# Kernel tuning notes

Hardware: AMD Instinct MI355X
Metric: run time of the kernel (lower is better)

The kernel has to match this reference:

```python
import jax, jax.numpy as jnp
import numpy as np

B, I, O, N = 65536, 256, 32, 8


def chebyshev_basis(x, n):
    """Chebyshev polynomials T_0..T_{n-1} of x. x: [B, I] -> [B, I, n]."""
    T = [jnp.ones_like(x), x]
    for _ in range(n - 2):
        T.append(2.0 * x * T[-1] - T[-2])
    return jnp.stack(T[:n], axis=-1)


def setup_inputs() -> dict:
    key = jax.random.key(0)
    k1, k2 = jax.random.split(key)
    # inputs live on [-1, 1], the natural Chebyshev domain
    x = jax.random.uniform(k1, (B, I), jnp.float32, minval=-1.0, maxval=1.0)
    # weight init mirrors torch: uniform(-weight_magnitude/in, weight_magnitude/in)
    w = jax.random.uniform(k2, (O, I, N), jnp.float32, minval=-1.0 / I, maxval=1.0 / I)
    return {"x": x, "w": w}


def reference(x, w):
    n = w.shape[-1]
    phi = chebyshev_basis(x, n)          # [B, I, n] basis expansion
    out = jnp.einsum("bin,oin->bo", phi, w)  # weighted contraction
    return out
```

## Files before the change

### kernel.cpp

```cpp
#include <hip/hip_runtime.h>
#include <hip/hip_bf16.h>


typedef __attribute__((ext_vector_type(8)))  short bf16x8;
typedef __attribute__((ext_vector_type(16))) float f32x16;
typedef __attribute__((ext_vector_type(4)))  float f32x4;

__device__ __forceinline__ short f2b(float f) {
    __hip_bfloat16 h = __float2bfloat16(f);
    short s;
    __builtin_memcpy(&s, &h, sizeof(s));
    return s;
}

__device__ __forceinline__ unsigned pkbf(float lo, float hi) {
    __hip_bfloat162 h2 = __float22bfloat162_rn(make_float2(lo, hi));
    unsigned u;
    __builtin_memcpy(&u, &h2, 4);
    return u;
}

__global__ __launch_bounds__(256) void prep_w_kernel(const float* __restrict__ w,
                                                     short* __restrict__ wB) {
    int idx = blockIdx.x * 256 + threadIdx.x;
    int kc2 = idx >> 9;
    int l   = (idx >> 3) & 63;
    int jj  = idx & 7;
    int o = l & 31, g = l >> 5;
    int i = 2 * kc2 + (jj >> 2);
    int n = 4 * g + (jj & 3);
    wB[idx] = f2b(w[(o * 256 + i) * 8 + n]);
}

__global__ __launch_bounds__(256, 5) void cheb_mm_kernel(const float* __restrict__ x,
                                                         const short* __restrict__ wB,
                                                         float* __restrict__ out) {
    __shared__ float smem[8192];
    const int tid = threadIdx.x;
    const int wv  = tid >> 6;
    const int l   = tid & 63;
    const int g   = l >> 5;
    const int r0  = l & 31;
    const long long rowB = (long long)blockIdx.x * 32;

    const bf16x8* wq = (const bf16x8*)wB + wv * 2048 + l;
    bf16x8 bfc[4];
    #pragma unroll
    for (int p = 0; p < 4; ++p) bfc[p] = wq[p * 64];

    {
        const float4* xg4 = (const float4*)(x + rowB * 256);
        const int f4l = l & 15;
        const int rsub = l >> 4;
        float4 stg[8];
        #pragma unroll
        for (int q = 0; q < 8; ++q)
            stg[q] = xg4[(q * 4 + rsub) * 64 + wv * 16 + f4l];
        #pragma unroll
        for (int q = 0; q < 8; ++q) {
            const int row  = q * 4 + rsub;
            const int base = row * 256 + wv * 64;
            const int s    = row & 31;
            const int p0 = 2 * f4l, p1 = 2 * f4l + 1;
            *(float2*)&smem[base + 2 * (p0 ^ s)] = make_float2(stg[q].x, stg[q].y);
            *(float2*)&smem[base + 2 * (p1 ^ s)] = make_float2(stg[q].z, stg[q].w);
        }
    }

    f32x16 accA{}, accB{};
    const float* sf = smem;
    const int xbase = r0 * 256 + wv * 64 + g;

    float xc[2];
    xc[0] = sf[xbase + ((0 ^ r0) << 1)];
    xc[1] = sf[xbase + ((1 ^ r0) << 1)];

    #pragma unroll
    for (int t = 0; t < 32; ++t) {
        const bf16x8 bfrag = bfc[t & 3];
        const float  xv    = xc[t & 1];
        if (t + 4 < 32) bfc[t & 3] = wq[(t + 4) * 64];
        if (t + 2 < 32) xc[t & 1] = sf[xbase + (((t + 2) ^ r0) << 1)];

        const float x2 = xv + xv;
        const float T2 = fmaf(x2, xv, -1.f);
        const float T3 = fmaf(x2, T2, -xv);
        const float T4 = fmaf(x2, T3, -T2);
        const float T5 = fmaf(x2, T4, -T3);
        const float T6 = fmaf(x2, T5, -T4);
        const float T7 = fmaf(x2, T6, -T5);
        unsigned R0 = pkbf(1.f, xv);
        unsigned R1 = pkbf(T2, T3);
        unsigned R2 = pkbf(T4, T5);
        unsigned R3 = pkbf(T6, T7);
        auto r02 = __builtin_amdgcn_permlane32_swap(R0, R2, false, false);
        auto r13 = __builtin_amdgcn_permlane32_swap(R1, R3, false, false);
        union { unsigned u[4]; bf16x8 v; } af;
        af.u[0] = r02[0]; af.u[1] = r13[0];
        af.u[2] = r02[1]; af.u[3] = r13[1];
        if (t & 1)
            accB = __builtin_amdgcn_mfma_f32_32x32x16_bf16(af.v, bfrag, accB, 0, 0, 0);
        else
            accA = __builtin_amdgcn_mfma_f32_32x32x16_bf16(af.v, bfrag, accA, 0, 0, 0);
    }
    const f32x16 acc = accA + accB;

    #pragma unroll
    for (int r = 0; r < 16; ++r) {
        const int rloc = (r & 3) + 8 * (r >> 2) + 4 * g;
        smem[rloc * 256 + wv * 64 + r0] = acc[r];
    }
    __syncthreads();

    {
        float* op = out + rowB * 32;
        const int f   = tid * 4;
        const int row = f >> 5;
        const int c   = f & 31;
        const int b   = row * 256 + c;
        f32x4 v0 = *(const f32x4*)&smem[b];
        f32x4 v1 = *(const f32x4*)&smem[b + 64];
        f32x4 v2 = *(const f32x4*)&smem[b + 128];
        f32x4 v3 = *(const f32x4*)&smem[b + 192];
        f32x4 s = (v0 + v1) + (v2 + v3);
        *(f32x4*)(op + f) = s;
    }
}

extern "C" void kernel_launch(void* const* d_in, const int* in_sizes, int n_in,
                              void* d_out, int out_size, void* d_ws, size_t ws_size,
                              hipStream_t stream) {
    const float* x = (const float*)d_in[0];
    const float* w = (const float*)d_in[1];
    float* out = (float*)d_out;
    short* wB = (short*)d_ws;

    prep_w_kernel<<<256, 256, 0, stream>>>(w, wB);
    cheb_mm_kernel<<<2048, 256, 0, stream>>>(x, wB, out);
}
```

Baseline: 31.05 us.

## Make matmul kernel persistent with double-buffered x tiles and register-resident weights

New measurement: 42.99 us. +38.5%, slower.

```diff
diff --git a/kernel.cpp b/kernel.cpp
--- a/kernel.cpp
+++ b/kernel.cpp
@@ -32,98 +32,114 @@
     wB[idx] = f2b(w[(o * 256 + i) * 8 + n]);
 }
 
-__global__ __launch_bounds__(256, 5) void cheb_mm_kernel(const float* __restrict__ x,
+__global__ __launch_bounds__(256, 2) void cheb_mm_kernel(const float* __restrict__ x,
                                                          const short* __restrict__ wB,
                                                          float* __restrict__ out) {
-    __shared__ float smem[8192];
+    __shared__ float smem[16384];
     const int tid = threadIdx.x;
     const int wv  = tid >> 6;
     const int l   = tid & 63;
     const int g   = l >> 5;
     const int r0  = l & 31;
-    const long long rowB = (long long)blockIdx.x * 32;
+    const int f4l = l & 15;
+    const int rsub = l >> 4;
 
-    const bf16x8* wq = (const bf16x8*)wB + wv * 2048 + l;
-    bf16x8 bfc[4];
-    #pragma unroll
-    for (int p = 0; p < 4; ++p) bfc[p] = wq[p * 64];
+    float4 stg[8];
 
-    {
-        const float4* xg4 = (const float4*)(x + rowB * 256);
-        const int f4l = l & 15;
-        const int rsub = l >> 4;
-        float4 stg[8];
+    auto LOADT = [&](int T) {
+        const float4* xg4 = (const float4*)x + (long long)T * 2048;
         #pragma unroll
         for (int q = 0; q < 8; ++q)
             stg[q] = xg4[(q * 4 + rsub) * 64 + wv * 16 + f4l];
+    };
+    auto WRITET = [&](int buf) {
         #pragma unroll
         for (int q = 0; q < 8; ++q) {
             const int row  = q * 4 + rsub;
-            const int base = row * 256 + wv * 64;
+            const int base = buf * 8192 + row * 256 + wv * 64;
             const int s    = row & 31;
             const int p0 = 2 * f4l, p1 = 2 * f4l + 1;
             *(float2*)&smem[base + 2 * (p0 ^ s)] = make_float2(stg[q].x, stg[q].y);
             *(float2*)&smem[base + 2 * (p1 ^ s)] = make_float2(stg[q].z, stg[q].w);
         }
-    }
+    };
 
-    f32x16 accA{}, accB{};
-    const float* sf = smem;
-    const int xbase = r0 * 256 + wv * 64 + g;
+    const int T0 = blockIdx.x;
 
-    float xc[2];
-    xc[0] = sf[xbase + ((0 ^ r0) << 1)];
-    xc[1] = sf[xbase + ((1 ^ r0) << 1)];
+    LOADT(T0);
 
+    const bf16x8* wq = (const bf16x8*)wB + wv * 2048 + l;
+    bf16x8 ball[32];
     #pragma unroll
-    for (int t = 0; t < 32; ++t) {
-        const bf16x8 bfrag = bfc[t & 3];
-        const float  xv    = xc[t & 1];
-        if (t + 4 < 32) bfc[t & 3] = wq[(t + 4) * 64];
-        if (t + 2 < 32) xc[t & 1] = sf[xbase + (((t + 2) ^ r0) << 1)];
+    for (int t = 0; t < 32; ++t) ball[t] = wq[t * 64];
 
-        const float x2 = xv + xv;
-        const float T2 = fmaf(x2, xv, -1.f);
-        const float T3 = fmaf(x2, T2, -xv);
-        const float T4 = fmaf(x2, T3, -T2);
-        const float T5 = fmaf(x2, T4, -T3);
-        const float T6 = fmaf(x2, T5, -T4);
-        const float T7 = fmaf(x2, T6, -T5);
-        unsigned R0 = pkbf(1.f, xv);
-        unsigned R1 = pkbf(T2, T3);
-        unsigned R2 = pkbf(T4, T5);
-        unsigned R3 = pkbf(T6, T7);
-        auto r02 = __builtin_amdgcn_permlane32_swap(R0, R2, false, false);
-        auto r13 = __builtin_amdgcn_permlane32_swap(R1, R3, false, false);
-        union { unsigned u[4]; bf16x8 v; } af;
-        af.u[0] = r02[0]; af.u[1] = r13[0];
-        af.u[2] = r02[1]; af.u[3] = r13[1];
-        if (t & 1)
-            accB = __builtin_amdgcn_mfma_f32_32x32x16_bf16(af.v, bfrag, accB, 0, 0, 0);
-        else
-            accA = __builtin_amdgcn_mfma_f32_32x32x16_bf16(af.v, bfrag, accA, 0, 0, 0);
-    }
-    const f32x16 acc = accA + accB;
+    WRITET(0);
 
-    #pragma unroll
-    for (int r = 0; r < 16; ++r) {
-        const int rloc = (r & 3) + 8 * (r >> 2) + 4 * g;
-        smem[rloc * 256 + wv * 64 + r0] = acc[r];
-    }
-    __syncthreads();
+    for (int tt = 0; tt < 4; ++tt) {
+        const int p = tt & 1;
+        const long long rowB = (long long)(T0 + 512 * tt) * 32;
 
-    {
-        float* op = out + rowB * 32;
-        const int f   = tid * 4;
-        const int row = f >> 5;
-        const int c   = f & 31;
-        const int b   = row * 256 + c;
-        f32x4 v0 = *(const f32x4*)&smem[b];
-        f32x4 v1 = *(const f32x4*)&smem[b + 64];
-        f32x4 v2 = *(const f32x4*)&smem[b + 128];
-        f32x4 v3 = *(const f32x4*)&smem[b + 192];
-        f32x4 s = (v0 + v1) + (v2 + v3);
-        *(f32x4*)(op + f) = s;
+        if (tt < 3) LOADT(T0 + 512 * (tt + 1));
+
+        f32x16 accA{}, accB{};
+        const float* sf = smem + p * 8192;
+        const int xbase = r0 * 256 + wv * 64 + g;
+        float xc[2];
+        xc[0] = sf[xbase + ((0 ^ r0) << 1)];
+        xc[1] = sf[xbase + ((1 ^ r0) << 1)];
+
+        #pragma unroll
+        for (int t = 0; t < 32; ++t) {
+            const bf16x8 bfrag = ball[t];
+            const float  xv    = xc[t & 1];
+            if (t + 2 < 32) xc[t & 1] = sf[xbase + (((t + 2) ^ r0) << 1)];
+
+            const float x2 = xv + xv;
+            const float T2 = fmaf(x2, xv, -1.f);
+            const float T3 = fmaf(x2, T2, -xv);
+            const float T4 = fmaf(x2, T3, -T2);
+            const float T5 = fmaf(x2, T4, -T3);
+            const float T6 = fmaf(x2, T5, -T4);
+            const float T7 = fmaf(x2, T6, -T5);
+            unsigned R0 = pkbf(1.f, xv);
+            unsigned R1 = pkbf(T2, T3);
+            unsigned R2 = pkbf(T4, T5);
+            unsigned R3 = pkbf(T6, T7);
+            auto r02 = __builtin_amdgcn_permlane32_swap(R0, R2, false, false);
+            auto r13 = __builtin_amdgcn_permlane32_swap(R1, R3, false, false);
+            union { unsigned u[4]; bf16x8 v; } af;
+            af.u[0] = r02[0]; af.u[1] = r13[0];
+            af.u[2] = r02[1]; af.u[3] = r13[1];
+            if (t & 1)
+                accB = __builtin_amdgcn_mfma_f32_32x32x16_bf16(af.v, bfrag, accB, 0, 0, 0);
+            else
+                accA = __builtin_amdgcn_mfma_f32_32x32x16_bf16(af.v, bfrag, accA, 0, 0, 0);
+        }
+        const f32x16 acc = accA + accB;
+
+        #pragma unroll
+        for (int r = 0; r < 16; ++r) {
+            const int rloc = (r & 3) + 8 * (r >> 2) + 4 * g;
+            smem[p * 8192 + rloc * 256 + wv * 64 + r0] = acc[r];
+        }
+        __syncthreads();
+
+        {
+            float* op = out + rowB * 32;
+            const int f   = tid * 4;
+            const int row = f >> 5;
+            const int c   = f & 31;
+            const int b   = p * 8192 + row * 256 + c;
+            f32x4 v0 = *(const f32x4*)&smem[b];
+            f32x4 v1 = *(const f32x4*)&smem[b + 64];
+            f32x4 v2 = *(const f32x4*)&smem[b + 128];
+            f32x4 v3 = *(const f32x4*)&smem[b + 192];
+            f32x4 s = (v0 + v1) + (v2 + v3);
+            *(f32x4*)(op + f) = s;
+        }
+        __syncthreads();
+
+        if (tt < 3) WRITET(p ^ 1);
     }
 }
 
@@ -136,5 +152,5 @@
     short* wB = (short*)d_ws;
 
     prep_w_kernel<<<256, 256, 0, stream>>>(w, wB);
-    cheb_mm_kernel<<<2048, 256, 0, stream>>>(x, wB, out);
+    cheb_mm_kernel<<<512, 256, 0, stream>>>(x, wB, out);
 }
```
